# Performance work log

Hardware: AMD Instinct MI355X
Metric: run time of the kernel (lower is better)

Reference implementation:

```python
import jax, jax.numpy as jnp
import numpy as np

CHUNK = 512  # points per scan step; keeps per-step (B,CHUNK,M) dist tile ~64MB

def _nn_min_sqdist(x, y):
    """Per-point squared distance to nearest neighbor.
    x: (B,N,3), y: (B,M,3) -> (B,N). Chunked over N to avoid a full (B,N,M) matrix.
    """
    B, N, D = x.shape
    y2 = jnp.sum(y * y, axis=-1)  # (B,M)
    nchunks = N // CHUNK
    xc = x.reshape(B, nchunks, CHUNK, D).transpose(1, 0, 2, 3)  # (nchunks,B,C,D)

    def body(carry, xck):  # xck: (B,C,D)
        x2 = jnp.sum(xck * xck, axis=-1)  # (B,C)
        d = x2[:, :, None] + y2[:, None, :] - 2.0 * jnp.einsum('bcd,bmd->bcm', xck, y)
        return carry, jnp.min(d, axis=-1)  # (B,C)

    _, mins = jax.lax.scan(body, None, xc)  # (nchunks,B,C)
    return mins.transpose(1, 0, 2).reshape(B, N)


def setup_inputs() -> dict:
    key = jax.random.key(0)
    k1, k2 = jax.random.split(key)
    pred = jax.random.normal(k1, (4, 8192, 3), dtype=jnp.float32)
    gt = jax.random.normal(k2, (4, 8192, 3), dtype=jnp.float32)
    return {"pred": pred, "gt": gt}


def reference(pred, gt):
    beta, gamma, delta = 1.0, 1.0, 0.0  # ChamferLoss defaults; threshold=None, percentage=1.0
    N = pred.shape[1]
    pred2gt = _nn_min_sqdist(pred, gt)  # (B,N)
    gt2pred = _nn_min_sqdist(gt, pred)  # (B,M)
    loss = (jnp.mean(pred2gt, axis=-1)
            + jnp.mean(gt2pred, axis=-1) * (delta * N + gamma)
            + jnp.max(pred2gt, axis=-1) * beta)
    return jnp.mean(loss)
```

## Files before the change

kernel.cpp:

```cpp
#include <hip/hip_runtime.h>


typedef short  s16x8  __attribute__((ext_vector_type(8)));
typedef float  f32x16 __attribute__((ext_vector_type(16)));

#define BATCH 4
#define NPTS  8192
#define TPB   256
#define YS    4
#define YPS   (NPTS / YS)
#define STPTS 1024
#define STTILES (STPTS / 32)
#define XPB   256
#define NXC   (NPTS / XPB)
#define RBLK  64

__device__ __forceinline__ unsigned int bft(float f) { return __float_as_uint(f) >> 16; }
__device__ __forceinline__ float bfv(unsigned int s) { return __uint_as_float(s << 16); }

__device__ __forceinline__ void yfrag(float a0, float a1, float a2,
                                      uint4& w0, uint4& w1) {
    const unsigned int yh0 = bft(a0), yh1 = bft(a1), yh2 = bft(a2);
    const float l0 = a0 - bfv(yh0), l1 = a1 - bfv(yh1), l2 = a2 - bfv(yh2);
    const unsigned int nh0 = bft(-2.f * bfv(yh0));
    const unsigned int nh1 = bft(-2.f * bfv(yh1));
    const unsigned int nh2 = bft(-2.f * bfv(yh2));
    const unsigned int nl0 = bft(-2.f * l0), nl1 = bft(-2.f * l1), nl2 = bft(-2.f * l2);
    const float y2 = a0 * a0 + a1 * a1 + a2 * a2;
    const unsigned int q2h = bft(y2);
    const unsigned int q2l = bft(y2 - bfv(q2h));
    w0.x = nh0 | (nh1 << 16);
    w0.y = nh2 | (nl0 << 16);
    w0.z = nl1 | (nl2 << 16);
    w0.w = nh0 | (nh1 << 16);
    w1.x = nh2 | (q2h << 16);
    w1.y = q2l;
    w1.z = 0u; w1.w = 0u;
}

__global__ __launch_bounds__(TPB, 4)
void nn_fused(const float* __restrict__ pred, const float* __restrict__ gt,
              float* __restrict__ pmin, unsigned int* __restrict__ accum) {
    const int xc = blockIdx.x, sl = blockIdx.y, bd = blockIdx.z;
    const int t = threadIdx.x;
    if (xc == 0 && sl == 0 && bd == 0 && t < 17) accum[t] = 0u;

    const int b = bd >> 1, dir = bd & 1;
    const float* xp = (dir ? gt : pred) + (size_t)b * NPTS * 3;
    const float* yp = (dir ? pred : gt) + (size_t)b * NPTS * 3;

    const int w = t >> 6, l = t & 63;
    const int m32 = l & 31, hh = l >> 5;
    const int xbase = xc * XPB + w * 64;

    __shared__ uint4 ldsb[STTILES * 64];

    s16x8 af[2];
    float x2j[2];
    #pragma unroll
    for (int j = 0; j < 2; ++j) {
        const int xi = xbase + j * 32 + m32;
        const float c0 = xp[xi * 3], c1 = xp[xi * 3 + 1], c2 = xp[xi * 3 + 2];
        x2j[j] = c0 * c0 + c1 * c1 + c2 * c2;
        const unsigned int xh0 = bft(c0), xh1 = bft(c1), xh2 = bft(c2);
        const unsigned int xl0 = bft(c0 - bfv(xh0));
        const unsigned int xl1 = bft(c1 - bfv(xh1));
        const unsigned int xl2 = bft(c2 - bfv(xh2));
        s16x8 a;
        a[0] = (short)(hh ? xl2 : xh0);
        a[1] = (short)(hh ? 0x3F80u : xh1);
        a[2] = (short)(hh ? 0x3F80u : xh2);
        a[3] = (short)(hh ? 0u : xh0);
        a[4] = (short)(hh ? 0u : xh1);
        a[5] = (short)(hh ? 0u : xh2);
        a[6] = (short)(hh ? 0u : xl0);
        a[7] = (short)(hh ? 0u : xl1);
        af[j] = a;
    }

    f32x16 zero, mn0, mn1;
    #pragma unroll
    for (int r = 0; r < 16; ++r) { zero[r] = 0.f; mn0[r] = 3.4e38f; mn1[r] = 3.4e38f; }

    const uint4* bp = ldsb + l;

    for (int s = 0; s < 2; ++s) {
        if (s) __syncthreads();
        #pragma unroll
        for (int i = 0; i < 4; ++i) {
            const int p = i * 256 + t;
            const int pt = sl * YPS + s * STPTS + p;
            const float a0 = yp[pt * 3], a1 = yp[pt * 3 + 1], a2 = yp[pt * 3 + 2];
            uint4 q0, q1;
            yfrag(a0, a1, a2, q0, q1);
            ldsb[(p >> 5) * 64 + (p & 31)]      = q0;
            ldsb[(p >> 5) * 64 + 32 + (p & 31)] = q1;
        }
        __syncthreads();
        #pragma unroll
        for (int tp = 0; tp < STTILES; tp += 2) {
            const s16x8 bfa = __builtin_bit_cast(s16x8, bp[tp * 64]);
            const s16x8 bfb = __builtin_bit_cast(s16x8, bp[(tp + 1) * 64]);
            const f32x16 e0a = __builtin_amdgcn_mfma_f32_32x32x16_bf16(af[0], bfa, zero, 0, 0, 0);
            const f32x16 e1a = __builtin_amdgcn_mfma_f32_32x32x16_bf16(af[1], bfa, zero, 0, 0, 0);
            const f32x16 e0b = __builtin_amdgcn_mfma_f32_32x32x16_bf16(af[0], bfb, zero, 0, 0, 0);
            const f32x16 e1b = __builtin_amdgcn_mfma_f32_32x32x16_bf16(af[1], bfb, zero, 0, 0, 0);
            #pragma unroll
            for (int r = 0; r < 16; ++r) {
                mn0[r] = fminf(fminf(mn0[r], e0a[r]), e0b[r]);
                mn1[r] = fminf(fminf(mn1[r], e1a[r]), e1b[r]);
            }
        }
    }

    #pragma unroll
    for (int off = 16; off; off >>= 1) {
        #pragma unroll
        for (int r = 0; r < 16; ++r) {
            mn0[r] = fminf(mn0[r], __shfl_xor(mn0[r], off, 64));
            mn1[r] = fminf(mn1[r], __shfl_xor(mn1[r], off, 64));
        }
    }

    const int r = l & 15;
    const int row = (r & 3) + 8 * (r >> 2) + 4 * hh;
    float v0 = mn0[0], v1 = mn1[0];
    #pragma unroll
    for (int rr = 1; rr < 16; ++rr) {
        v0 = (r == rr) ? mn0[rr] : v0;
        v1 = (r == rr) ? mn1[rr] : v1;
    }
    const float x20 = __shfl(x2j[0], row, 64);
    const float x21 = __shfl(x2j[1], row, 64);
    const bool g1 = (l & 31) >= 16;
    const float d = fmaxf((g1 ? v1 : v0) + (g1 ? x21 : x20), 0.f);
    const int xpt = xbase + (g1 ? 32 : 0) + row;
    pmin[((size_t)bd * YS + sl) * NPTS + xpt] = d;
}

__global__ __launch_bounds__(TPB)
void reduce_all(const float* __restrict__ pmin, float* __restrict__ accum,
                float* __restrict__ out) {
    const int g = blockIdx.x, bd = g >> 3, seg = g & 7;
    const int t = threadIdx.x;
    const float4* base = (const float4*)(pmin + (size_t)bd * YS * NPTS);
    const int f4 = seg * 256 + t;
    float4 q = base[f4];
    #pragma unroll
    for (int sl = 1; sl < YS; ++sl) {
        const float4 rr = base[sl * (NPTS / 4) + f4];
        q.x = fminf(q.x, rr.x); q.y = fminf(q.y, rr.y);
        q.z = fminf(q.z, rr.z); q.w = fminf(q.w, rr.w);
    }
    float s = (q.x + q.y) + (q.z + q.w);
    float m = fmaxf(fmaxf(q.x, q.y), fmaxf(q.z, q.w));
    #pragma unroll
    for (int off = 32; off; off >>= 1) {
        s += __shfl_down(s, off, 64);
        m = fmaxf(m, __shfl_down(m, off, 64));
    }
    __shared__ float ws_[4], wm_[4];
    if ((t & 63) == 0) { ws_[t >> 6] = s; wm_[t >> 6] = m; }
    __syncthreads();
    if (t == 0) {
        s = (ws_[0] + ws_[1]) + (ws_[2] + ws_[3]);
        m = fmaxf(fmaxf(wm_[0], wm_[1]), fmaxf(wm_[2], wm_[3]));
        atomicAdd(&accum[bd], s);
        atomicMax((unsigned int*)accum + 8 + bd, __float_as_uint(m));
        __threadfence();
        const unsigned int done = atomicAdd((unsigned int*)accum + 16, 1u);
        if (done == RBLK - 1) {
            float acc = 0.f;
            #pragma unroll
            for (int b2 = 0; b2 < BATCH; ++b2) {
                const float s0 = atomicAdd(&accum[2 * b2], 0.f);
                const float s1 = atomicAdd(&accum[2 * b2 + 1], 0.f);
                const unsigned int mb =
                    atomicMax((unsigned int*)accum + 8 + 2 * b2, 0u);
                acc += (s0 + s1) * (1.f / NPTS) + __uint_as_float(mb);
            }
            out[0] = acc * (1.f / BATCH);
        }
    }
}

extern "C" void kernel_launch(void* const* d_in, const int* in_sizes, int n_in,
                              void* d_out, int out_size, void* d_ws, size_t ws_size,
                              hipStream_t stream) {
    const float* pred = (const float*)d_in[0];
    const float* gt   = (const float*)d_in[1];

    float* pmin = (float*)d_ws;
    float* accum = (float*)((char*)d_ws + (size_t)2 * BATCH * YS * NPTS * 4);

    dim3 g1(NXC, YS, 2 * BATCH);
    nn_fused<<<g1, TPB, 0, stream>>>(pred, gt, pmin, (unsigned int*)accum);
    reduce_all<<<dim3(RBLK), TPB, 0, stream>>>(pmin, accum, (float*)d_out);
}
```

Baseline: 83.60 us.

## Switch to 16x16x32 MFMA with compact 16-byte y fragments in LDS

Replaces the 32x32x16 bf16 MFMA formulation with 16x16x32 tiles, packing each y point's hi/lo coordinates and squared norm into one 16-byte LDS entry instead of two. The whole y slice is now staged in LDS in a single pass, which removes the second staging round and its barrier. Each wave handles four 16-row x tiles instead of two 32-row tiles. This halves LDS footprint per point and K-padding waste, but the per-wave min reduction and store pattern change, and the larger LDS array may limit occupancy.

```diff
diff --git a/kernel.cpp b/kernel.cpp
--- a/kernel.cpp
+++ b/kernel.cpp
@@ -2,41 +2,20 @@
 
 
 typedef short  s16x8  __attribute__((ext_vector_type(8)));
-typedef float  f32x16 __attribute__((ext_vector_type(16)));
+typedef float  f32x4  __attribute__((ext_vector_type(4)));
 
 #define BATCH 4
 #define NPTS  8192
 #define TPB   256
 #define YS    4
 #define YPS   (NPTS / YS)
-#define STPTS 1024
-#define STTILES (STPTS / 32)
+#define YT16  (YPS / 16)
 #define XPB   256
 #define NXC   (NPTS / XPB)
 #define RBLK  64
 
 __device__ __forceinline__ unsigned int bft(float f) { return __float_as_uint(f) >> 16; }
 __device__ __forceinline__ float bfv(unsigned int s) { return __uint_as_float(s << 16); }
-
-__device__ __forceinline__ void yfrag(float a0, float a1, float a2,
-                                      uint4& w0, uint4& w1) {
-    const unsigned int yh0 = bft(a0), yh1 = bft(a1), yh2 = bft(a2);
-    const float l0 = a0 - bfv(yh0), l1 = a1 - bfv(yh1), l2 = a2 - bfv(yh2);
-    const unsigned int nh0 = bft(-2.f * bfv(yh0));
-    const unsigned int nh1 = bft(-2.f * bfv(yh1));
-    const unsigned int nh2 = bft(-2.f * bfv(yh2));
-    const unsigned int nl0 = bft(-2.f * l0), nl1 = bft(-2.f * l1), nl2 = bft(-2.f * l2);
-    const float y2 = a0 * a0 + a1 * a1 + a2 * a2;
-    const unsigned int q2h = bft(y2);
-    const unsigned int q2l = bft(y2 - bfv(q2h));
-    w0.x = nh0 | (nh1 << 16);
-    w0.y = nh2 | (nl0 << 16);
-    w0.z = nl1 | (nl2 << 16);
-    w0.w = nh0 | (nh1 << 16);
-    w1.x = nh2 | (q2h << 16);
-    w1.y = q2l;
-    w1.z = 0u; w1.w = 0u;
-}
 
 __global__ __launch_bounds__(TPB, 4)
 void nn_fused(const float* __restrict__ pred, const float* __restrict__ gt,
@@ -50,92 +29,109 @@
     const float* yp = (dir ? pred : gt) + (size_t)b * NPTS * 3;
 
     const int w = t >> 6, l = t & 63;
-    const int m32 = l & 31, hh = l >> 5;
+    const int c16 = l & 15, g = l >> 4;
     const int xbase = xc * XPB + w * 64;
 
-    __shared__ uint4 ldsb[STTILES * 64];
+    __shared__ uint4 ldsb[YPS];
 
-    s16x8 af[2];
-    float x2j[2];
+    s16x8 af[4];
+    float x2j[4];
     #pragma unroll
-    for (int j = 0; j < 2; ++j) {
-        const int xi = xbase + j * 32 + m32;
+    for (int xt = 0; xt < 4; ++xt) {
+        const int xi = xbase + xt * 16 + c16;
         const float c0 = xp[xi * 3], c1 = xp[xi * 3 + 1], c2 = xp[xi * 3 + 2];
-        x2j[j] = c0 * c0 + c1 * c1 + c2 * c2;
+        x2j[xt] = c0 * c0 + c1 * c1 + c2 * c2;
         const unsigned int xh0 = bft(c0), xh1 = bft(c1), xh2 = bft(c2);
         const unsigned int xl0 = bft(c0 - bfv(xh0));
         const unsigned int xl1 = bft(c1 - bfv(xh1));
         const unsigned int xl2 = bft(c2 - bfv(xh2));
+        const unsigned int s0 = (g == 0) ? xh0 : (g == 1 ? xl0 : 0u);
+        const unsigned int s1 = (g == 0) ? xh1 : (g == 1 ? xl1 : 0u);
+        const unsigned int s2 = (g == 0) ? xh2 : (g == 1 ? xl2 : 0u);
+        const unsigned int s3 = (g == 0) ? 0x3F80u : 0u;
         s16x8 a;
-        a[0] = (short)(hh ? xl2 : xh0);
-        a[1] = (short)(hh ? 0x3F80u : xh1);
-        a[2] = (short)(hh ? 0x3F80u : xh2);
-        a[3] = (short)(hh ? 0u : xh0);
-        a[4] = (short)(hh ? 0u : xh1);
-        a[5] = (short)(hh ? 0u : xh2);
-        a[6] = (short)(hh ? 0u : xl0);
-        a[7] = (short)(hh ? 0u : xl1);
-        af[j] = a;
+        a[0] = (short)s0; a[1] = (short)s1; a[2] = (short)s2;
+        a[3] = (short)s0; a[4] = (short)s1; a[5] = (short)s2;
+        a[6] = (short)s3; a[7] = (short)s3;
+        af[xt] = a;
     }
 
-    f32x16 zero, mn0, mn1;
     #pragma unroll
-    for (int r = 0; r < 16; ++r) { zero[r] = 0.f; mn0[r] = 3.4e38f; mn1[r] = 3.4e38f; }
+    for (int i = 0; i < 8; ++i) {
+        const int p = i * 256 + t;
+        const int pt = sl * YPS + p;
+        const float a0 = yp[pt * 3], a1 = yp[pt * 3 + 1], a2 = yp[pt * 3 + 2];
+        const unsigned int yh0 = bft(a0), yh1 = bft(a1), yh2 = bft(a2);
+        const float l0 = a0 - bfv(yh0), l1 = a1 - bfv(yh1), l2 = a2 - bfv(yh2);
+        const unsigned int nh0 = bft(-2.f * bfv(yh0));
+        const unsigned int nh1 = bft(-2.f * bfv(yh1));
+        const unsigned int nh2 = bft(-2.f * bfv(yh2));
+        const unsigned int nl0 = bft(-2.f * l0), nl1 = bft(-2.f * l1), nl2 = bft(-2.f * l2);
+        const float y2 = a0 * a0 + a1 * a1 + a2 * a2;
+        const unsigned int q2h = bft(y2);
+        const unsigned int q2l = bft(y2 - bfv(q2h));
+        uint4 w0;
+        w0.x = nh0 | (nh1 << 16);
+        w0.y = nh2 | (nl0 << 16);
+        w0.z = nl1 | (nl2 << 16);
+        w0.w = q2h | (q2l << 16);
+        ldsb[p] = w0;
+    }
+    __syncthreads();
 
-    const uint4* bp = ldsb + l;
+    f32x4 zero, mn[4];
+    #pragma unroll
+    for (int r = 0; r < 4; ++r) {
+        zero[r] = 0.f;
+        mn[0][r] = 3.4e38f; mn[1][r] = 3.4e38f; mn[2][r] = 3.4e38f; mn[3][r] = 3.4e38f;
+    }
 
-    for (int s = 0; s < 2; ++s) {
-        if (s) __syncthreads();
+    const uint4* bp = ldsb + c16;
+    for (int tp = 0; tp < YT16; tp += 4) {
         #pragma unroll
-        for (int i = 0; i < 4; ++i) {
-            const int p = i * 256 + t;
-            const int pt = sl * YPS + s * STPTS + p;
-            const float a0 = yp[pt * 3], a1 = yp[pt * 3 + 1], a2 = yp[pt * 3 + 2];
-            uint4 q0, q1;
-            yfrag(a0, a1, a2, q0, q1);
-            ldsb[(p >> 5) * 64 + (p & 31)]      = q0;
-            ldsb[(p >> 5) * 64 + 32 + (p & 31)] = q1;
-        }
-        __syncthreads();
-        #pragma unroll
-        for (int tp = 0; tp < STTILES; tp += 2) {
-            const s16x8 bfa = __builtin_bit_cast(s16x8, bp[tp * 64]);
-            const s16x8 bfb = __builtin_bit_cast(s16x8, bp[(tp + 1) * 64]);
-            const f32x16 e0a = __builtin_amdgcn_mfma_f32_32x32x16_bf16(af[0], bfa, zero, 0, 0, 0);
-            const f32x16 e1a = __builtin_amdgcn_mfma_f32_32x32x16_bf16(af[1], bfa, zero, 0, 0, 0);
-            const f32x16 e0b = __builtin_amdgcn_mfma_f32_32x32x16_bf16(af[0], bfb, zero, 0, 0, 0);
-            const f32x16 e1b = __builtin_amdgcn_mfma_f32_32x32x16_bf16(af[1], bfb, zero, 0, 0, 0);
+        for (int u = 0; u < 2; ++u) {
+            const s16x8 bfa = __builtin_bit_cast(s16x8, bp[(tp + 2 * u) * 16]);
+            const s16x8 bfb = __builtin_bit_cast(s16x8, bp[(tp + 2 * u + 1) * 16]);
             #pragma unroll
-            for (int r = 0; r < 16; ++r) {
-                mn0[r] = fminf(fminf(mn0[r], e0a[r]), e0b[r]);
-                mn1[r] = fminf(fminf(mn1[r], e1a[r]), e1b[r]);
+            for (int xt = 0; xt < 4; ++xt) {
+                const f32x4 ea = __builtin_amdgcn_mfma_f32_16x16x32_bf16(af[xt], bfa, zero, 0, 0, 0);
+                const f32x4 eb = __builtin_amdgcn_mfma_f32_16x16x32_bf16(af[xt], bfb, zero, 0, 0, 0);
+                #pragma unroll
+                for (int r = 0; r < 4; ++r)
+                    mn[xt][r] = fminf(fminf(mn[xt][r], ea[r]), eb[r]);
             }
         }
     }
 
     #pragma unroll
-    for (int off = 16; off; off >>= 1) {
+    for (int off = 8; off; off >>= 1) {
         #pragma unroll
-        for (int r = 0; r < 16; ++r) {
-            mn0[r] = fminf(mn0[r], __shfl_xor(mn0[r], off, 64));
-            mn1[r] = fminf(mn1[r], __shfl_xor(mn1[r], off, 64));
-        }
+        for (int xt = 0; xt < 4; ++xt)
+            #pragma unroll
+            for (int r = 0; r < 4; ++r)
+                mn[xt][r] = fminf(mn[xt][r], __shfl_xor(mn[xt][r], off, 64));
     }
 
-    const int r = l & 15;
-    const int row = (r & 3) + 8 * (r >> 2) + 4 * hh;
-    float v0 = mn0[0], v1 = mn1[0];
-    #pragma unroll
-    for (int rr = 1; rr < 16; ++rr) {
-        v0 = (r == rr) ? mn0[rr] : v0;
-        v1 = (r == rr) ? mn1[rr] : v1;
+    const int cr = l & 3;
+    const float x2s0 = __shfl(x2j[0], g * 4 + cr, 64);
+    const float x2s1 = __shfl(x2j[1], g * 4 + cr, 64);
+    const float x2s2 = __shfl(x2j[2], g * 4 + cr, 64);
+    const float x2s3 = __shfl(x2j[3], g * 4 + cr, 64);
+    if (c16 < 4) {
+        float v0 = mn[0][0], v1 = mn[1][0], v2 = mn[2][0], v3 = mn[3][0];
+        #pragma unroll
+        for (int rr = 1; rr < 4; ++rr) {
+            v0 = (cr == rr) ? mn[0][rr] : v0;
+            v1 = (cr == rr) ? mn[1][rr] : v1;
+            v2 = (cr == rr) ? mn[2][rr] : v2;
+            v3 = (cr == rr) ? mn[3][rr] : v3;
+        }
+        float* dst = pmin + ((size_t)bd * YS + sl) * NPTS + xbase + g * 4 + cr;
+        dst[0]  = fmaxf(v0 + x2s0, 0.f);
+        dst[16] = fmaxf(v1 + x2s1, 0.f);
+        dst[32] = fmaxf(v2 + x2s2, 0.f);
+        dst[48] = fmaxf(v3 + x2s3, 0.f);
     }
-    const float x20 = __shfl(x2j[0], row, 64);
-    const float x21 = __shfl(x2j[1], row, 64);
-    const bool g1 = (l & 31) >= 16;
-    const float d = fmaxf((g1 ? v1 : v0) + (g1 ? x21 : x20), 0.f);
-    const int xpt = xbase + (g1 ? 32 : 0) + row;
-    pmin[((size_t)bd * YS + sl) * NPTS + xpt] = d;
 }
 
 __global__ __launch_bounds__(TPB)
```

Result: slower. 86.73 us (+3.7%).
